# Kernel tuning notes

Measured on AMD Instinct MI355X. Metric: run time of the kernel, lower is better.

## Reference

```python
import jax, jax.numpy as jnp
import numpy as np


def setup_inputs() -> dict:
    key = jax.random.key(0)
    ks = jax.random.split(key, 8)
    B, Cq, Ckv, Co, T, H, W = 2, 256, 256, 256, 8, 28, 28
    s = 1.0 / np.sqrt(Cq)
    return {
        "x": jax.random.normal(ks[0], (B, Cq, T, H, W), jnp.float32),
        "context": jax.random.normal(ks[1], (B, Ckv, T, H, W), jnp.float32),
        "wq": jax.random.normal(ks[2], (Co, Cq), jnp.float32) * s,
        "bq": jnp.zeros((Co,), jnp.float32),
        "wk": jax.random.normal(ks[3], (Co, Ckv), jnp.float32) * s,
        "bk": jnp.zeros((Co,), jnp.float32),
        "wv": jax.random.normal(ks[4], (Co, Ckv), jnp.float32) * s,
        "bv": jnp.zeros((Co,), jnp.float32),
    }


def reference(x, context, wq, bq, wk, bk, wv, bv):
    B, C, T, H, W = x.shape
    N = T * H * W
    Co = wq.shape[0]
    # 1x1x1 Conv3d == per-voxel linear projection over channels
    def proj(inp, w, b):
        y = jnp.einsum('bcthw,oc->bothw', inp, w) + b[None, :, None, None, None]
        return y.reshape(B, Co, N)  # [B, Co, N]
    q = proj(x, wq, bq).transpose(0, 2, 1)        # [B, N, Co]
    k = proj(context, wk, bk)                     # [B, Co, Nc]
    v = proj(context, wv, bv).transpose(0, 2, 1)  # [B, Nc, Co]
    scale = 1.0 / jnp.sqrt(jnp.asarray(Co, x.dtype))
    attn = jax.nn.softmax(jnp.einsum('bnc,bcm->bnm', q, k) * scale, axis=-1)
    out = jnp.einsum('bnm,bmc->bnc', attn, v)     # [B, N, Co]
    out = out.transpose(0, 2, 1).reshape(B, Co, T, H, W)
    return out + x
```

## Files before the change

### kernel.cpp

```cpp
#include <hip/hip_runtime.h>
#include <hip/hip_bf16.h>
#include <math.h>

#define BB 2
#define CC 256
#define NN 6272
#define NT32 196
#define NKB32 196
#define SCL 0.09016844005f

typedef __attribute__((ext_vector_type(8))) short s8v;
typedef __attribute__((ext_vector_type(4))) float f4v;
typedef __attribute__((ext_vector_type(4))) unsigned short us4v;

__device__ inline unsigned short f2bf(float f) {
  unsigned u = __builtin_bit_cast(unsigned, f);
  u += 0x7fffu + ((u >> 16) & 1u);
  return (unsigned short)(u >> 16);
}

__device__ inline float bf2f(unsigned short h) {
  unsigned u = (unsigned)h << 16;
  return __builtin_bit_cast(float, u);
}

__global__ __launch_bounds__(256) void wcvt_kernel(
    const float* __restrict__ wq, const float* __restrict__ wk,
    const float* __restrict__ wv, unsigned short* __restrict__ Wb)
{
  int i = (blockIdx.x * 256 + threadIdx.x) * 4;
  const float* src = (i < 65536) ? wq : (i < 131072 ? wk : wv);
  int off = i & 65535;
  float4 v = *(const float4*)(src + off);
  ushort4 o;
  o.x = f2bf(v.x); o.y = f2bf(v.y); o.z = f2bf(v.z); o.w = f2bf(v.w);
  *(ushort4*)(Wb + i) = o;
}

__global__ __launch_bounds__(256) void proj_kernel(
    const float* __restrict__ x, const float* __restrict__ ctx,
    const unsigned short* __restrict__ Wb,
    const float* __restrict__ bq, const float* __restrict__ bk,
    const float* __restrict__ bv,
    unsigned short* __restrict__ Q, unsigned short* __restrict__ Kk,
    unsigned short* __restrict__ V)
{
  const int p = blockIdx.z, b = blockIdx.y;
  const int n0 = blockIdx.x * 32;
  const int tid = threadIdx.x;
  const float* in = (p == 0 ? x : ctx) + (size_t)b * CC * NN;
  const unsigned short* W = Wb + (size_t)p * 65536;
  const float* bias = (p == 0 ? bq : (p == 1 ? bk : bv));

  __shared__ __align__(16) unsigned short lds[32][264];
  for (int it = tid; it < 2048; it += 256) {
    int c  = it >> 3;
    int n4 = (it & 7) << 2;
    float4 v = *(const float4*)(in + (size_t)c * NN + n0 + n4);
    lds[n4 + 0][c] = f2bf(v.x);
    lds[n4 + 1][c] = f2bf(v.y);
    lds[n4 + 2][c] = f2bf(v.z);
    lds[n4 + 3][c] = f2bf(v.w);
  }
  __syncthreads();

  const int lane = tid & 63, l15 = lane & 15, g = lane >> 4;
  const int obase = (tid >> 6) * 64;

  f4v acc[4][2];
#pragma unroll
  for (int mt = 0; mt < 4; ++mt) {
    float4 b4 = *(const float4*)(bias + obase + mt * 16 + g * 4);
    f4v bi = {b4.x, b4.y, b4.z, b4.w};
    acc[mt][0] = bi; acc[mt][1] = bi;
  }

#pragma unroll
  for (int ks = 0; ks < 8; ++ks) {
    s8v bf0 = *(const s8v*)(&lds[l15][ks * 32 + g * 8]);
    s8v bf1 = *(const s8v*)(&lds[16 + l15][ks * 32 + g * 8]);
#pragma unroll
    for (int mt = 0; mt < 4; ++mt) {
      s8v wa = *(const s8v*)(W + (size_t)(obase + mt * 16 + l15) * CC + ks * 32 + g * 8);
      acc[mt][0] = __builtin_amdgcn_mfma_f32_16x16x32_bf16(wa, bf0, acc[mt][0], 0, 0, 0);
      acc[mt][1] = __builtin_amdgcn_mfma_f32_16x16x32_bf16(wa, bf1, acc[mt][1], 0, 0, 0);
    }
  }

  if (p == 0) {
#pragma unroll
    for (int mt = 0; mt < 4; ++mt)
#pragma unroll
      for (int qq = 0; qq < 2; ++qq)
#pragma unroll
        for (int r = 0; r < 4; ++r)
          acc[mt][qq][r] *= SCL;
  }

  if (p < 2) {
    unsigned short* dst = (p == 0 ? Q : Kk) + (size_t)b * NN * CC;
#pragma unroll
    for (int mt = 0; mt < 4; ++mt)
#pragma unroll
      for (int qq = 0; qq < 2; ++qq) {
        ushort4 pk;
        pk.x = f2bf(acc[mt][qq][0]); pk.y = f2bf(acc[mt][qq][1]);
        pk.z = f2bf(acc[mt][qq][2]); pk.w = f2bf(acc[mt][qq][3]);
        *(ushort4*)(dst + (size_t)(n0 + qq * 16 + l15) * CC + obase + mt * 16 + g * 4) = pk;
      }
  } else {
    unsigned short* dstb = V + (size_t)b * CC * NN;
#pragma unroll
    for (int mt = 0; mt < 4; ++mt)
#pragma unroll
      for (int qq = 0; qq < 2; ++qq)
#pragma unroll
        for (int r = 0; r < 4; ++r)
          dstb[(size_t)(obase + mt * 16 + g * 4 + r) * NN + n0 + qq * 16 + l15] =
              f2bf(acc[mt][qq][r]);
  }
}

__global__ __launch_bounds__(256, 2) void attn_kernel(
    const unsigned short* __restrict__ Qg,
    const unsigned short* __restrict__ Kg,
    const unsigned short* __restrict__ Vg,
    unsigned short* __restrict__ Opart,
    float* __restrict__ ml,
    int split, int kb_base, int kb_rem)
{
  const int s     = blockIdx.x % split;
  const int stile = blockIdx.x / split;
  const int b     = stile / 49;
  const int qsup  = stile % 49;
  const int tid   = threadIdx.x;
  const int w     = tid >> 6;
  const int lane  = tid & 63;
  const int l15 = lane & 15, g = lane >> 4;
  const int qt32  = qsup * 4 + w;
  const int q0    = qt32 * 32;
  const int wid32 = b * NT32 + qt32;

  const int start = s * kb_base + (s < kb_rem ? s : kb_rem);
  const int cnt   = kb_base + (s < kb_rem ? 1 : 0);

  const unsigned short* Qb = Qg + (size_t)b * NN * CC;
  const unsigned short* Kb = Kg + (size_t)b * NN * CC;
  const unsigned short* Vb = Vg + (size_t)b * CC * NN;

  __shared__ __align__(16) unsigned short K_lds[2][32 * 256];
  __shared__ __align__(16) unsigned short V_lds[2][256 * 32];
  __shared__ __align__(16) unsigned short P_lds[4][2][16][36];

  s8v qf[2][8];
#pragma unroll
  for (int qt = 0; qt < 2; ++qt)
#pragma unroll
    for (int ks = 0; ks < 8; ++ks)
      qf[qt][ks] = *(const s8v*)(Qb + (size_t)(q0 + qt * 16 + l15) * CC + ks * 32 + g * 8);

  f4v ot[2][16];
  const f4v fz = {0.f, 0.f, 0.f, 0.f};
#pragma unroll
  for (int qt = 0; qt < 2; ++qt)
#pragma unroll
    for (int mt = 0; mt < 16; ++mt) ot[qt][mt] = fz;

  float lsum[2] = {0.f, 0.f};

  auto stage = [&](int buf, int kb32) {
    const int kb = kb32 * 32;
#pragma unroll
    for (int i = 0; i < 8; ++i) {
      int chunk = w * 512 + i * 64 + lane;
      if (chunk < 1024) {
        int r = chunk >> 5, cc = chunk & 31;
        const unsigned short* gp =
            Kb + (size_t)(kb + r) * CC + ((cc ^ (r & 15)) << 3);
        __builtin_amdgcn_global_load_lds(
            (const __attribute__((address_space(1))) unsigned int*)gp,
            (__attribute__((address_space(3))) unsigned int*)(&K_lds[buf][chunk * 8]),
            16, 0, 0);
      } else {
        int vc = chunk - 1024;
        int ch = vc >> 2, cc = vc & 3;
        const unsigned short* gp =
            Vb + (size_t)ch * NN + kb + ((cc ^ ((ch >> 1) & 3)) << 3);
        __builtin_amdgcn_global_load_lds(
            (const __attribute__((address_space(1))) unsigned int*)gp,
            (__attribute__((address_space(3))) unsigned int*)(&V_lds[buf][vc * 8]),
            16, 0, 0);
      }
    }
  };

  stage(0, start);
  int cur = 0;

  for (int ib = 0; ib < cnt; ++ib) {
    __syncthreads();
    if (ib + 1 < cnt) stage(cur ^ 1, start + ib + 1);

    const unsigned short* Kl = &K_lds[cur][0];
    const unsigned short* Vl = &V_lds[cur][0];

    f4v st[2][2];
    st[0][0] = fz; st[0][1] = fz; st[1][0] = fz; st[1][1] = fz;
#pragma unroll
    for (int ks = 0; ks < 8; ++ks) {
      const int co = ((ks * 4 + g) ^ l15) << 3;
      s8v ka0 = *(const s8v*)(Kl + (l15) * 256 + co);
      s8v ka1 = *(const s8v*)(Kl + (16 + l15) * 256 + co);
      st[0][0] = __builtin_amdgcn_mfma_f32_16x16x32_bf16(ka0, qf[0][ks], st[0][0], 0, 0, 0);
      st[0][1] = __builtin_amdgcn_mfma_f32_16x16x32_bf16(ka0, qf[1][ks], st[0][1], 0, 0, 0);
      st[1][0] = __builtin_amdgcn_mfma_f32_16x16x32_bf16(ka1, qf[0][ks], st[1][0], 0, 0, 0);
      st[1][1] = __builtin_amdgcn_mfma_f32_16x16x32_bf16(ka1, qf[1][ks], st[1][1], 0, 0, 0);
    }

#pragma unroll
    for (int kt = 0; kt < 2; ++kt)
#pragma unroll
      for (int qt = 0; qt < 2; ++qt) {
        float p0 = __builtin_amdgcn_exp2f(st[kt][qt][0]);
        float p1 = __builtin_amdgcn_exp2f(st[kt][qt][1]);
        float p2 = __builtin_amdgcn_exp2f(st[kt][qt][2]);
        float p3 = __builtin_amdgcn_exp2f(st[kt][qt][3]);
        lsum[qt] += (p0 + p1) + (p2 + p3);
        ushort4 pk;
        pk.x = f2bf(p0); pk.y = f2bf(p1); pk.z = f2bf(p2); pk.w = f2bf(p3);
        *(ushort4*)(&P_lds[w][qt][l15][kt * 16 + 4 * g]) = pk;
      }

    s8v pb0 = *(const s8v*)(&P_lds[w][0][l15][g * 8]);
    s8v pb1 = *(const s8v*)(&P_lds[w][1][l15][g * 8]);
    const int vo = (g ^ ((l15 >> 1) & 3)) << 3;
#pragma unroll
    for (int mt = 0; mt < 16; ++mt) {
      s8v va = *(const s8v*)(Vl + (mt * 16 + l15) * 32 + vo);
      ot[0][mt] = __builtin_amdgcn_mfma_f32_16x16x32_bf16(va, pb0, ot[0][mt], 0, 0, 0);
      ot[1][mt] = __builtin_amdgcn_mfma_f32_16x16x32_bf16(va, pb1, ot[1][mt], 0, 0, 0);
    }

    cur ^= 1;
  }

#pragma unroll
  for (int qt = 0; qt < 2; ++qt) {
    lsum[qt] += __shfl_xor(lsum[qt], 16);
    lsum[qt] += __shfl_xor(lsum[qt], 32);
  }

  unsigned short* Ob = Opart + (size_t)(wid32 * split + s) * 8192;
#pragma unroll
  for (int qt = 0; qt < 2; ++qt)
#pragma unroll
    for (int mt = 0; mt < 16; ++mt) {
      us4v o4;
      o4.x = f2bf(ot[qt][mt][0]); o4.y = f2bf(ot[qt][mt][1]);
      o4.z = f2bf(ot[qt][mt][2]); o4.w = f2bf(ot[qt][mt][3]);
      __builtin_nontemporal_store(o4, (us4v*)(Ob + qt * 4096 + mt * 256 + lane * 4));
    }

  if (lane < 16) {
    ml[(size_t)(wid32 * split + s) * 32 + lane]      = lsum[0];
    ml[(size_t)(wid32 * split + s) * 32 + 16 + lane] = lsum[1];
  }
}

__global__ __launch_bounds__(256) void merge_kernel(
    const unsigned short* __restrict__ Opart,
    const float* __restrict__ ml,
    const float* __restrict__ x,
    float* __restrict__ out,
    int split)
{
  const int wid32 = blockIdx.x;
  const int b  = wid32 / NT32;
  const int pi = wid32 % NT32;
  const int n0 = pi * 32;
  const int tid = threadIdx.x;
  const int w = tid >> 6;
  const int lane = tid & 63;
  const int l15 = lane & 15, g = lane >> 4;

  __shared__ float lds_o[256][33];

#pragma unroll
  for (int t = 0; t < 2; ++t) {
    float L = 0.f;
#pragma unroll
    for (int s = 0; s < 8; ++s)
      if (s < split)
        L += ml[(size_t)(wid32 * split + s) * 32 + t * 16 + l15];
    const float invL = 1.f / L;

#pragma unroll
    for (int j = 0; j < 4; ++j) {
      int mt = j * 4 + w;
      float a0 = 0.f, a1 = 0.f, a2 = 0.f, a3 = 0.f;
#pragma unroll
      for (int s = 0; s < 8; ++s)
        if (s < split) {
          const us4v* Op4 = (const us4v*)(Opart +
              (size_t)(wid32 * split + s) * 8192 + t * 4096);
          us4v o4 = __builtin_nontemporal_load(Op4 + mt * 64 + lane);
          a0 += bf2f(o4.x); a1 += bf2f(o4.y);
          a2 += bf2f(o4.z); a3 += bf2f(o4.w);
        }
      int c = mt * 16 + g * 4;
      int nl = t * 16 + l15;
      lds_o[c + 0][nl] = a0 * invL;
      lds_o[c + 1][nl] = a1 * invL;
      lds_o[c + 2][nl] = a2 * invL;
      lds_o[c + 3][nl] = a3 * invL;
    }
  }
  __syncthreads();

  const size_t base = (size_t)b * CC * NN + n0;
  const int n = tid & 31;
  const int c0 = tid >> 5;
#pragma unroll
  for (int cg = 0; cg < 32; ++cg) {
    int c = cg * 8 + c0;
    size_t idx = base + (size_t)c * NN + n;
    out[idx] = lds_o[c][n] + x[idx];
  }
}

extern "C" void kernel_launch(void* const* d_in, const int* in_sizes, int n_in,
                              void* d_out, int out_size, void* d_ws, size_t ws_size,
                              hipStream_t stream) {
  const float* x   = (const float*)d_in[0];
  const float* ctx = (const float*)d_in[1];
  const float* wq  = (const float*)d_in[2];
  const float* bq  = (const float*)d_in[3];
  const float* wk  = (const float*)d_in[4];
  const float* bk  = (const float*)d_in[5];
  const float* wv  = (const float*)d_in[6];
  const float* bv  = (const float*)d_in[7];
  float* out = (float*)d_out;

  const size_t sz = (size_t)BB * NN * CC;
  unsigned short* Wb = (unsigned short*)d_ws;
  unsigned short* Q  = Wb + 3 * 65536;
  unsigned short* K  = Q + sz;
  unsigned short* V  = K + sz;
  const size_t fixedB = 3 * 65536 * 2 + 3 * sz * 2;

  int split = 1;
  const int cands[3] = {5, 2, 1};
  for (int i = 0; i < 3; ++i) {
    size_t need = fixedB + (size_t)cands[i] * (BB * NT32) *
                  (8192 * sizeof(unsigned short) + 32 * sizeof(float));
    if (ws_size >= need) { split = cands[i]; break; }
  }
  unsigned short* Opart = (unsigned short*)((char*)d_ws + fixedB);
  float* ml = (float*)(Opart + (size_t)split * (BB * NT32) * 8192);
  const int kb_base = NKB32 / split, kb_rem = NKB32 % split;

  wcvt_kernel<<<dim3(192), dim3(256), 0, stream>>>(wq, wk, wv, Wb);
  proj_kernel<<<dim3(NN / 32, BB, 3), dim3(256), 0, stream>>>(
      x, ctx, Wb, bq, bk, bv, Q, K, V);
  attn_kernel<<<dim3(98 * split), dim3(256), 0, stream>>>(
      Q, K, V, Opart, ml, split, kb_base, kb_rem);
  merge_kernel<<<dim3(BB * NT32), dim3(256), 0, stream>>>(
      Opart, ml, x, out, split);
}
```

Before: 285.7 us.

## Split each 32-query tile across two waves by key half and output channels

Each block now serves two 32-query tiles instead of four. Each wave pair shares a tile: one wave handles 16 of the 32 keys in each chunk and half of the 256 output channels. This halves the output accumulator registers per wave and doubles the grid, aiming for better occupancy and more blocks in flight. The cost is a block-wide barrier each iteration so the two halves can exchange P through LDS, plus duplicated Q fragment loads and extra partial row-sum entries for the merge kernel to add up.

```diff
diff --git a/kernel.cpp b/kernel.cpp
--- a/kernel.cpp
+++ b/kernel.cpp
@@ -131,15 +131,16 @@
 {
   const int s     = blockIdx.x % split;
   const int stile = blockIdx.x / split;
-  const int b     = stile / 49;
-  const int qsup  = stile % 49;
+  const int b     = stile / 98;
+  const int qsup  = stile % 98;
   const int tid   = threadIdx.x;
   const int w     = tid >> 6;
+  const int pr    = w >> 1;
+  const int h     = w & 1;
   const int lane  = tid & 63;
   const int l15 = lane & 15, g = lane >> 4;
-  const int qt32  = qsup * 4 + w;
-  const int q0    = qt32 * 32;
-  const int wid32 = b * NT32 + qt32;
+  const int wid32 = b * NT32 + qsup * 2 + pr;
+  const int q0    = (qsup * 2 + pr) * 32;
 
   const int start = s * kb_base + (s < kb_rem ? s : kb_rem);
   const int cnt   = kb_base + (s < kb_rem ? 1 : 0);
@@ -150,7 +151,7 @@
 
   __shared__ __align__(16) unsigned short K_lds[2][32 * 256];
   __shared__ __align__(16) unsigned short V_lds[2][256 * 32];
-  __shared__ __align__(16) unsigned short P_lds[4][2][16][36];
+  __shared__ __align__(16) unsigned short P_lds[2][32][40];
 
   s8v qf[2][8];
 #pragma unroll
@@ -159,12 +160,12 @@
     for (int ks = 0; ks < 8; ++ks)
       qf[qt][ks] = *(const s8v*)(Qb + (size_t)(q0 + qt * 16 + l15) * CC + ks * 32 + g * 8);
 
-  f4v ot[2][16];
+  f4v ot[2][8];
   const f4v fz = {0.f, 0.f, 0.f, 0.f};
 #pragma unroll
   for (int qt = 0; qt < 2; ++qt)
 #pragma unroll
-    for (int mt = 0; mt < 16; ++mt) ot[qt][mt] = fz;
+    for (int mt = 0; mt < 8; ++mt) ot[qt][mt] = fz;
 
   float lsum[2] = {0.f, 0.f};
 
@@ -204,39 +205,39 @@
     const unsigned short* Kl = &K_lds[cur][0];
     const unsigned short* Vl = &V_lds[cur][0];
 
-    f4v st[2][2];
-    st[0][0] = fz; st[0][1] = fz; st[1][0] = fz; st[1][1] = fz;
+    f4v st[2];
+    st[0] = fz; st[1] = fz;
 #pragma unroll
     for (int ks = 0; ks < 8; ++ks) {
       const int co = ((ks * 4 + g) ^ l15) << 3;
-      s8v ka0 = *(const s8v*)(Kl + (l15) * 256 + co);
-      s8v ka1 = *(const s8v*)(Kl + (16 + l15) * 256 + co);
-      st[0][0] = __builtin_amdgcn_mfma_f32_16x16x32_bf16(ka0, qf[0][ks], st[0][0], 0, 0, 0);
-      st[0][1] = __builtin_amdgcn_mfma_f32_16x16x32_bf16(ka0, qf[1][ks], st[0][1], 0, 0, 0);
-      st[1][0] = __builtin_amdgcn_mfma_f32_16x16x32_bf16(ka1, qf[0][ks], st[1][0], 0, 0, 0);
-      st[1][1] = __builtin_amdgcn_mfma_f32_16x16x32_bf16(ka1, qf[1][ks], st[1][1], 0, 0, 0);
-    }
-
-#pragma unroll
-    for (int kt = 0; kt < 2; ++kt)
-#pragma unroll
-      for (int qt = 0; qt < 2; ++qt) {
-        float p0 = __builtin_amdgcn_exp2f(st[kt][qt][0]);
-        float p1 = __builtin_amdgcn_exp2f(st[kt][qt][1]);
-        float p2 = __builtin_amdgcn_exp2f(st[kt][qt][2]);
-        float p3 = __builtin_amdgcn_exp2f(st[kt][qt][3]);
-        lsum[qt] += (p0 + p1) + (p2 + p3);
-        ushort4 pk;
-        pk.x = f2bf(p0); pk.y = f2bf(p1); pk.z = f2bf(p2); pk.w = f2bf(p3);
-        *(ushort4*)(&P_lds[w][qt][l15][kt * 16 + 4 * g]) = pk;
-      }
-
-    s8v pb0 = *(const s8v*)(&P_lds[w][0][l15][g * 8]);
-    s8v pb1 = *(const s8v*)(&P_lds[w][1][l15][g * 8]);
+      s8v ka = *(const s8v*)(Kl + (h * 16 + l15) * 256 + co);
+      st[0] = __builtin_amdgcn_mfma_f32_16x16x32_bf16(ka, qf[0][ks], st[0], 0, 0, 0);
+      st[1] = __builtin_amdgcn_mfma_f32_16x16x32_bf16(ka, qf[1][ks], st[1], 0, 0, 0);
+    }
+
+#pragma unroll
+    for (int qt = 0; qt < 2; ++qt) {
+      float p0 = __builtin_amdgcn_exp2f(st[qt][0]);
+      float p1 = __builtin_amdgcn_exp2f(st[qt][1]);
+      float p2 = __builtin_amdgcn_exp2f(st[qt][2]);
+      float p3 = __builtin_amdgcn_exp2f(st[qt][3]);
+      lsum[qt] += (p0 + p1) + (p2 + p3);
+      ushort4 pk;
+      pk.x = f2bf(p0); pk.y = f2bf(p1); pk.z = f2bf(p2); pk.w = f2bf(p3);
+      *(ushort4*)(&P_lds[pr][qt * 16 + l15][h * 16 + g * 4]) = pk;
+    }
+
+    __builtin_amdgcn_sched_barrier(0);
+    asm volatile("s_waitcnt lgkmcnt(0)" ::: "memory");
+    __builtin_amdgcn_s_barrier();
+    __builtin_amdgcn_sched_barrier(0);
+
+    s8v pb0 = *(const s8v*)(&P_lds[pr][l15][g * 8]);
+    s8v pb1 = *(const s8v*)(&P_lds[pr][16 + l15][g * 8]);
     const int vo = (g ^ ((l15 >> 1) & 3)) << 3;
 #pragma unroll
-    for (int mt = 0; mt < 16; ++mt) {
-      s8v va = *(const s8v*)(Vl + (mt * 16 + l15) * 32 + vo);
+    for (int mt = 0; mt < 8; ++mt) {
+      s8v va = *(const s8v*)(Vl + (h * 128 + mt * 16 + l15) * 32 + vo);
       ot[0][mt] = __builtin_amdgcn_mfma_f32_16x16x32_bf16(va, pb0, ot[0][mt], 0, 0, 0);
       ot[1][mt] = __builtin_amdgcn_mfma_f32_16x16x32_bf16(va, pb1, ot[1][mt], 0, 0, 0);
     }
@@ -254,16 +255,17 @@
 #pragma unroll
   for (int qt = 0; qt < 2; ++qt)
 #pragma unroll
-    for (int mt = 0; mt < 16; ++mt) {
+    for (int mt = 0; mt < 8; ++mt) {
       us4v o4;
       o4.x = f2bf(ot[qt][mt][0]); o4.y = f2bf(ot[qt][mt][1]);
       o4.z = f2bf(ot[qt][mt][2]); o4.w = f2bf(ot[qt][mt][3]);
-      __builtin_nontemporal_store(o4, (us4v*)(Ob + qt * 4096 + mt * 256 + lane * 4));
+      __builtin_nontemporal_store(
+          o4, (us4v*)(Ob + qt * 4096 + (h * 8 + mt) * 256 + lane * 4));
     }
 
   if (lane < 16) {
-    ml[(size_t)(wid32 * split + s) * 32 + lane]      = lsum[0];
-    ml[(size_t)(wid32 * split + s) * 32 + 16 + lane] = lsum[1];
+    ml[(size_t)(wid32 * split + s) * 64 + h * 32 + lane]      = lsum[0];
+    ml[(size_t)(wid32 * split + s) * 64 + h * 32 + 16 + lane] = lsum[1];
   }
 }
 
@@ -290,8 +292,10 @@
     float L = 0.f;
 #pragma unroll
     for (int s = 0; s < 8; ++s)
-      if (s < split)
-        L += ml[(size_t)(wid32 * split + s) * 32 + t * 16 + l15];
+      if (s < split) {
+        L += ml[(size_t)(wid32 * split + s) * 64 + t * 16 + l15];
+        L += ml[(size_t)(wid32 * split + s) * 64 + 32 + t * 16 + l15];
+      }
     const float invL = 1.f / L;
 
 #pragma unroll
@@ -352,7 +356,7 @@
   const int cands[3] = {5, 2, 1};
   for (int i = 0; i < 3; ++i) {
     size_t need = fixedB + (size_t)cands[i] * (BB * NT32) *
-                  (8192 * sizeof(unsigned short) + 32 * sizeof(float));
+                  (8192 * sizeof(unsigned short) + 64 * sizeof(float));
     if (ws_size >= need) { split = cands[i]; break; }
   }
   unsigned short* Opart = (unsigned short*)((char*)d_ws + fixedB);
@@ -362,7 +366,7 @@
   wcvt_kernel<<<dim3(192), dim3(256), 0, stream>>>(wq, wk, wv, Wb);
   proj_kernel<<<dim3(NN / 32, BB, 3), dim3(256), 0, stream>>>(
       x, ctx, Wb, bq, bk, bv, Q, K, V);
-  attn_kernel<<<dim3(98 * split), dim3(256), 0, stream>>>(
+  attn_kernel<<<dim3(196 * split), dim3(256), 0, stream>>>(
       Q, K, V, Opart, ml, split, kb_base, kb_rem);
   merge_kernel<<<dim3(BB * NT32), dim3(256), 0, stream>>>(
       Opart, ml, x, out, split);
```

After: 254.3 us. 11.0% less time.
